# Kernel optimization log

Measured on AMD Instinct MI355X. Metric: run time of the kernel, lower is better.

## Reference

```python
import jax, jax.numpy as jnp
import numpy as np
from jax.scipy.linalg import expm

B, S, D, E, K, NROT = 2, 2048, 1024, 8, 2, 3
EPS = 1e-5


def setup_inputs() -> dict:
    key = jax.random.key(0)
    ks = jax.random.split(key, 16)
    sc = 0.02
    x = jax.random.normal(ks[0], (B, S, D), jnp.float32)
    ln_gamma = 1.0 + sc * jax.random.normal(ks[1], (D,), jnp.float32)
    ln_beta = sc * jax.random.normal(ks[2], (D,), jnp.float32)
    abel_w = sc * jax.random.normal(ks[3], (D, D), jnp.float32)
    abel_b = sc * jax.random.normal(ks[4], (D,), jnp.float32)
    moe_gate_w = sc * jax.random.normal(ks[5], (D, E), jnp.float32)
    moe_gate_b = sc * jax.random.normal(ks[6], (E,), jnp.float32)
    ew1 = sc * jax.random.normal(ks[7], (E, D, 2 * D), jnp.float32)
    eb1 = sc * jax.random.normal(ks[8], (E, 2 * D), jnp.float32)
    ew2 = sc * jax.random.normal(ks[9], (E, 2 * D, D), jnp.float32)
    eb2 = sc * jax.random.normal(ks[10], (E, D), jnp.float32)
    g = sc * jax.random.normal(ks[11], (NROT, D, D), jnp.float32)
    gens = 0.5 * (g - jnp.swapaxes(g, -1, -2))  # skew-symmetric, as in reset_parameters
    gc_w = sc * jax.random.normal(ks[12], (2 * D, 1), jnp.float32)
    gc_b = sc * jax.random.normal(ks[13], (1,), jnp.float32)
    return dict(x=x, ln_gamma=ln_gamma, ln_beta=ln_beta, abel_w=abel_w, abel_b=abel_b,
                moe_gate_w=moe_gate_w, moe_gate_b=moe_gate_b, ew1=ew1, eb1=eb1,
                ew2=ew2, eb2=eb2, gens=gens, gc_w=gc_w, gc_b=gc_b)


def _gelu(x):
    return jax.nn.gelu(x, approximate=False)  # torch nn.GELU default = exact erf


def _forward(x, ln_gamma, ln_beta, abel_w, abel_b, moe_gate_w, moe_gate_b,
             ew1, eb1, ew2, eb2, gens, gc_w, gc_b):
    residual = x
    # LayerNorm
    mu = jnp.mean(x, axis=-1, keepdims=True)
    var = jnp.mean((x - mu) ** 2, axis=-1, keepdims=True)
    xn = (x - mu) * jax.lax.rsqrt(var + EPS) * ln_gamma + ln_beta
    # abel branch: Linear + GELU
    abel_out = _gelu(xn @ abel_w + abel_b)
    # MoE: dense all-experts compute, masked by top-k softmax weights
    logits = xn @ moe_gate_w + moe_gate_b                      # [B,S,E]
    topw, topi = jax.lax.top_k(logits, K)                      # [B,S,K]
    topw = jax.nn.softmax(topw, axis=-1)
    w_dense = jnp.sum(jax.nn.one_hot(topi, E, dtype=xn.dtype) * topw[..., None], axis=-2)  # [B,S,E]
    h = _gelu(jnp.einsum('bsd,edh->ebsh', xn, ew1) + eb1[:, None, None, :])  # [E,B,S,2D]
    eo = jnp.einsum('ebsh,ehd->ebsd', h, ew2) + eb2[:, None, None, :]        # [E,B,S,D]
    moe_out = jnp.einsum('ebsd,bse->bsd', eo, w_dense)
    # GeometricRotation: sequential matrix_exp rotations
    for i in range(NROT):
        moe_out = moe_out @ expm(gens[i])
    # gated residual mix
    combined = jnp.concatenate([abel_out, moe_out], axis=-1)
    gate = jax.nn.sigmoid(combined @ gc_w + gc_b)              # [B,S,1]
    mixed = abel_out * (1.0 - gate) + moe_out * gate
    return residual + mixed


def reference(x, ln_gamma, ln_beta, abel_w, abel_b, moe_gate_w, moe_gate_b,
              ew1, eb1, ew2, eb2, gens, gc_w, gc_b):
    return _forward(x, ln_gamma, ln_beta, abel_w, abel_b, moe_gate_w, moe_gate_b,
                    ew1, eb1, ew2, eb2, gens, gc_w, gc_b)
```

## Files before the change

### kernel.cpp

```cpp
#include <hip/hip_runtime.h>
#include <hip/hip_bf16.h>
#include <cstdint>
#include <cstddef>

#define DD   1024
#define DD2  2048
#define EE   8
#define NTOK 4096
#define CAPR 9216

typedef __bf16 bf16_t;
typedef __bf16 bf16x8 __attribute__((ext_vector_type(8)));
typedef __bf16 bf16x4 __attribute__((ext_vector_type(4)));
typedef float  f32x4v __attribute__((ext_vector_type(4)));

__device__ __forceinline__ float gelu_f(float v){
  return 0.5f*v*(1.0f + erff(v*0.70710678118654752440f));
}

__device__ __forceinline__ void gload_lds16(const void* g, void* l){
  __builtin_amdgcn_global_load_lds(
    (const __attribute__((address_space(1))) unsigned int*)(uintptr_t)g,
    (__attribute__((address_space(3))) unsigned int*)(uintptr_t)l,
    16, 0, 0);
}

enum { EPI_GELU_F32=0, EPI_GELU_BF16=1, EPI_BIAS_BF16=2, EPI_SCALE_BF16=3,
       EPI_ADDV_BF16=4, EPI_BF16=5, EPI_F32=6 };

template<int BM,int BN,int EPI,bool DYN>
__global__ __launch_bounds__(256)
void gemm_bt(const bf16_t* __restrict__ A, const bf16_t* __restrict__ Bt,
             const bf16_t* __restrict__ Bt2,
             const int N, const int K, const int gx, const int gy, const int gz,
             const long sAz, const long sBz, const long sOz, const int zsplit,
             const int* __restrict__ cnt, const int* __restrict__ offp,
             const float* __restrict__ bias, const long sBias,
             const float alpha, const float alpha2,
             const bf16_t* __restrict__ addv,
             float* __restrict__ outF, bf16_t* __restrict__ outB)
{
  constexpr int BK = 64;
  constexpr int WM = BM/2, WN = BN/2;
  constexpr int FM = WM/16, FN = WN/16;
  constexpr int IA = BM/32, IB = BN/32;
  __shared__ alignas(16) bf16_t sA[BM*BK];
  __shared__ alignas(16) bf16_t sB[BN*BK];

  int bx, by, bz;
  if constexpr (DYN) {
    const int e = blockIdx.x & 7;
    const int i = blockIdx.x >> 3;
    bz = e; by = i / gx; bx = i - by*gx;
    if (by * BM >= cnt[e]) return;
  } else {
    const int nwg = gx * gy * gz;
    const int q = nwg >> 3, r = nwg & 7;
    const int k = blockIdx.x & 7, i = blockIdx.x >> 3;
    if (i >= q + (k < r ? 1 : 0)) return;
    const int l = k * q + (k < r ? k : r) + i;
    bx = l % gx; const int t2 = l / gx; by = t2 % gy; bz = t2 / gy;
  }

  const int z = bz;
  int zz = z; const bf16_t* Bp = Bt; float al = alpha;
  if (z >= zsplit) { zz = z - zsplit; Bp = Bt2; al = alpha2; }

  float*  oF = outF;
  bf16_t* oB = outB;
  if constexpr (DYN) {
    const long ro = offp[z];
    A  += ro * (long)K;
    oB += ro * (long)N;
  } else {
    A += (size_t)zz * sAz;
    if (oF) oF += (size_t)z * sOz;
    if (oB) oB += (size_t)z * sOz;
  }
  Bp += (size_t)zz * sBz;
  const float*  bp = bias ? bias + (size_t)z * sBias : nullptr;
  const bf16_t* vp = addv ? addv + (size_t)z * sOz   : nullptr;

  const int tid = threadIdx.x;
  const int wid = tid >> 6, lid = tid & 63;
  const int wr = wid >> 1, wc = wid & 1;
  const int brow = by * BM, bcol = bx * BN;
  const int sr = lid >> 3, sq = lid & 7;
  const int fr = lid & 15, fq = lid >> 4;

  f32x4v acc[FM][FN] = {};

  for (int kt = 0; kt < K; kt += BK) {
    #pragma unroll
    for (int i = 0; i < IA; i++) {
      const int ii = wid*IA + i;
      const int r  = ii*8 + sr;
      const int q  = sq ^ (r & 7);
      gload_lds16((const char*)A + ((size_t)(brow + r)*K + kt)*2 + q*16,
                  (char*)sA + ii*1024);
    }
    #pragma unroll
    for (int i = 0; i < IB; i++) {
      const int ii = wid*IB + i;
      const int r  = ii*8 + sr;
      const int q  = sq ^ (r & 7);
      gload_lds16((const char*)Bp + ((size_t)(bcol + r)*K + kt)*2 + q*16,
                  (char*)sB + ii*1024);
    }
    __syncthreads();

    #pragma unroll
    for (int kk = 0; kk < 2; kk++) {
      bf16x8 af[FM], bb[FN];
      #pragma unroll
      for (int mi = 0; mi < FM; mi++) {
        const int r = wr*WM + mi*16 + fr;
        const int q = (kk*4 + fq) ^ (r & 7);
        af[mi] = *(const bf16x8*)((const char*)sA + r*128 + q*16);
      }
      #pragma unroll
      for (int ni = 0; ni < FN; ni++) {
        const int r = wc*WN + ni*16 + fr;
        const int q = (kk*4 + fq) ^ (r & 7);
        bb[ni] = *(const bf16x8*)((const char*)sB + r*128 + q*16);
      }
      #pragma unroll
      for (int mi = 0; mi < FM; mi++)
        #pragma unroll
        for (int ni = 0; ni < FN; ni++)
          acc[mi][ni] = __builtin_amdgcn_mfma_f32_16x16x32_bf16(
              af[mi], bb[ni], acc[mi][ni], 0, 0, 0);
    }
    __syncthreads();
  }

  #pragma unroll
  for (int mi = 0; mi < FM; mi++) {
    #pragma unroll
    for (int ni = 0; ni < FN; ni++) {
      const int rg0 = brow + wr*WM + mi*16 + fq*4;
      const int cg  = bcol + wc*WN + ni*16 + fr;
      #pragma unroll
      for (int i = 0; i < 4; i++) {
        const int rg = rg0 + i;
        float v = acc[mi][ni][i];
        if constexpr (EPI == EPI_GELU_F32) {
          v += bp[cg];
          oF[(size_t)rg*N + cg] = gelu_f(v);
        } else if constexpr (EPI == EPI_GELU_BF16) {
          v += bp[cg];
          oB[(size_t)rg*N + cg] = (bf16_t)gelu_f(v);
        } else if constexpr (EPI == EPI_BIAS_BF16) {
          v += bp[cg];
          oB[(size_t)rg*N + cg] = (bf16_t)v;
        } else if constexpr (EPI == EPI_SCALE_BF16) {
          oB[(size_t)rg*N + cg] = (bf16_t)(v * al);
        } else if constexpr (EPI == EPI_ADDV_BF16) {
          oB[(size_t)rg*N + cg] = (bf16_t)(v + (float)vp[(size_t)rg*N + cg]);
        } else if constexpr (EPI == EPI_BF16) {
          oB[(size_t)rg*N + cg] = (bf16_t)v;
        } else {
          oF[(size_t)rg*N + cg] = v;
        }
      }
    }
  }
}

__global__ __launch_bounds__(256)
void tcvt_kernel(const float* __restrict__ src, bf16_t* __restrict__ dst, int R, int C){
  __shared__ float tile[32][33];
  const size_t bo = (size_t)blockIdx.z * R * C;
  const int c0 = blockIdx.x*32, r0 = blockIdx.y*32;
  #pragma unroll
  for (int i = 0; i < 4; i++) {
    const int r = r0 + threadIdx.y + i*8;
    tile[threadIdx.y + i*8][threadIdx.x] = src[bo + (size_t)r*C + c0 + threadIdx.x];
  }
  __syncthreads();
  #pragma unroll
  for (int i = 0; i < 4; i++) {
    const int c = c0 + threadIdx.y + i*8;
    dst[bo + (size_t)c*R + r0 + threadIdx.x] = (bf16_t)tile[threadIdx.x][threadIdx.y + i*8];
  }
}

__global__ __launch_bounds__(256)
void tb16_kernel(const bf16_t* __restrict__ Ut, bf16_t* __restrict__ Tb){
  __shared__ bf16_t tile[32][33];
  const bf16_t* src = Ut + (size_t)(1 - blockIdx.z) * DD * DD;
  bf16_t*       dst = Tb + (size_t)blockIdx.z * DD * DD;
  const int c0 = blockIdx.x*32, r0 = blockIdx.y*32;
  #pragma unroll
  for (int i = 0; i < 4; i++)
    tile[threadIdx.y + i*8][threadIdx.x] = src[(size_t)(r0 + threadIdx.y + i*8)*DD + c0 + threadIdx.x];
  __syncthreads();
  #pragma unroll
  for (int i = 0; i < 4; i++)
    dst[(size_t)(c0 + threadIdx.y + i*8)*DD + r0 + threadIdx.x] = tile[threadIdx.x][threadIdx.y + i*8];
}

__global__ __launch_bounds__(256)
void cvt_kernel(const float* __restrict__ in, bf16_t* __restrict__ o, long n, float scale){
  const long i = ((long)blockIdx.x*256 + threadIdx.x)*4;
  if (i >= n) return;
  const float4 v = *(const float4*)(in + i);
  bf16x4 b; b[0]=(bf16_t)(v.x*scale); b[1]=(bf16_t)(v.y*scale);
  b[2]=(bf16_t)(v.z*scale); b[3]=(bf16_t)(v.w*scale);
  *(bf16x4*)(o + i) = b;
}

__global__ __launch_bounds__(256)
void vw_kernel(const bf16_t* __restrict__ Hn, const bf16_t* __restrict__ H2,
               const bf16_t* __restrict__ H3, bf16_t* __restrict__ Vb,
               bf16_t* __restrict__ Wtb){
  const long i0 = ((long)blockIdx.x*256 + threadIdx.x)*4;
  const long rc = i0 % (long)(DD*DD);
  const int r = (int)(rc / DD), c0 = (int)(rc % DD);
  const bf16x4 h  = *(const bf16x4*)(Hn + i0);
  const bf16x4 h2 = *(const bf16x4*)(H2 + i0);
  const bf16x4 h3 = *(const bf16x4*)(H3 + i0);
  bf16x4 v, w;
  #pragma unroll
  for (int j = 0; j < 4; j++) {
    const float d  = (r == c0 + j) ? 1.0f : 0.0f;
    const float fh = (float)h[j], f2 = (float)h2[j], f3 = (float)h3[j];
    v[j] = (bf16_t)(d + fh + f2*0.5f + f3*(1.0f/6.0f));
    w[j] = (bf16_t)(d*(1.0f/24.0f) - fh*(1.0f/120.0f) + f2*(1.0f/720.0f) - f3*(1.0f/5040.0f));
  }
  *(bf16x4*)(Vb  + i0) = v;
  *(bf16x4*)(Wtb + i0) = w;
}

__global__ __launch_bounds__(256)
void ln_gate_kernel(const float* __restrict__ x, const float* __restrict__ gamma,
                    const float* __restrict__ beta, const float* __restrict__ gw,
                    const float* __restrict__ gb,
                    bf16_t* __restrict__ xnb, int2* __restrict__ ids,
                    float2* __restrict__ wts)
{
  const int t = blockIdx.x, tid = threadIdx.x, j0 = tid*4;
  const int wid = tid >> 6, lid = tid & 63;
  const float4 v = *(const float4*)(x + (size_t)t*DD + j0);
  float s  = v.x + v.y + v.z + v.w;
  float ss = v.x*v.x + v.y*v.y + v.z*v.z + v.w*v.w;
  #pragma unroll
  for (int off = 32; off; off >>= 1) { s += __shfl_down(s, off); ss += __shfl_down(ss, off); }
  __shared__ float redS[4], redQ[4], mv[2];
  if (lid == 0) { redS[wid] = s; redQ[wid] = ss; }
  __syncthreads();
  if (tid == 0) {
    const float S1 = redS[0]+redS[1]+redS[2]+redS[3];
    const float S2 = redQ[0]+redQ[1]+redQ[2]+redQ[3];
    const float mu  = S1 * (1.0f/DD);
    const float var = S2 * (1.0f/DD) - mu*mu;
    mv[0] = mu; mv[1] = rsqrtf(var + 1e-5f);
  }
  __syncthreads();
  const float mu = mv[0], rstd = mv[1];
  const float4 g = *(const float4*)(gamma + j0);
  const float4 b = *(const float4*)(beta  + j0);
  float xn[4];
  xn[0] = (v.x-mu)*rstd*g.x + b.x;
  xn[1] = (v.y-mu)*rstd*g.y + b.y;
  xn[2] = (v.z-mu)*rstd*g.z + b.z;
  xn[3] = (v.w-mu)*rstd*g.w + b.w;
  bf16x4 ov; ov[0]=(bf16_t)xn[0]; ov[1]=(bf16_t)xn[1]; ov[2]=(bf16_t)xn[2]; ov[3]=(bf16_t)xn[3];
  *(bf16x4*)(xnb + (size_t)t*DD + j0) = ov;

  float p[8] = {0,0,0,0,0,0,0,0};
  #pragma unroll
  for (int i = 0; i < 4; i++) {
    const float4 a0 = *(const float4*)(gw + (size_t)(j0+i)*EE);
    const float4 a1 = *(const float4*)(gw + (size_t)(j0+i)*EE + 4);
    const float xv = xn[i];
    p[0]+=xv*a0.x; p[1]+=xv*a0.y; p[2]+=xv*a0.z; p[3]+=xv*a0.w;
    p[4]+=xv*a1.x; p[5]+=xv*a1.y; p[6]+=xv*a1.z; p[7]+=xv*a1.w;
  }
  #pragma unroll
  for (int off = 32; off; off >>= 1) {
    #pragma unroll
    for (int e = 0; e < 8; e++) p[e] += __shfl_down(p[e], off);
  }
  __shared__ float pr[32];
  if (lid == 0) {
    #pragma unroll
    for (int e = 0; e < 8; e++) pr[wid*8 + e] = p[e];
  }
  __syncthreads();
  if (tid == 0) {
    float l[8];
    #pragma unroll
    for (int e = 0; e < 8; e++) l[e] = pr[e] + pr[8+e] + pr[16+e] + pr[24+e] + gb[e];
    int i1 = 0; float m1 = l[0];
    #pragma unroll
    for (int e = 1; e < 8; e++) if (l[e] > m1) { m1 = l[e]; i1 = e; }
    int i2 = 0; float m2 = -1e30f;
    #pragma unroll
    for (int e = 0; e < 8; e++) if (e != i1 && l[e] > m2) { m2 = l[e]; i2 = e; }
    const float wa = 1.0f/(1.0f + expf(m2 - m1));
    ids[t] = make_int2(i1, i2);
    wts[t] = make_float2(wa, 1.0f - wa);
  }
}

__global__ __launch_bounds__(256)
void route_kernel(const int2* __restrict__ ids, int* __restrict__ slotA,
                  int* __restrict__ slotB, int* __restrict__ cnt)
{
  const int e = blockIdx.x;
  const int tid = threadIdx.x;
  const int wid = tid >> 6, lid = tid & 63;
  __shared__ int wsum[4];
  int base = 0;
  const unsigned long long lt = (1ull << lid) - 1ull;
  for (int c0 = 0; c0 < NTOK; c0 += 256) {
    const int t = c0 + tid;
    const int2 id = ids[t];
    const bool fA = (id.x == e), fB = (id.y == e);
    const unsigned long long mA = __ballot(fA);
    const unsigned long long mB = __ballot(fB);
    const int cA = __popcll(mA), cB = __popcll(mB);
    const int pA = __popcll(mA & lt), pB = __popcll(mB & lt);
    if (lid == 0) wsum[wid] = cA + cB;
    __syncthreads();
    int wbase = 0;
    #pragma unroll
    for (int w = 0; w < 4; w++) if (w < wid) wbase += wsum[w];
    const int tot = wsum[0] + wsum[1] + wsum[2] + wsum[3];
    if (fA) slotA[t] = base + wbase + pA;
    if (fB) slotB[t] = base + wbase + cA + pB;
    base += tot;
    __syncthreads();
  }
  if (tid == 0) cnt[e] = base;
}

__global__ void offs_kernel(const int* __restrict__ cnt, int* __restrict__ off){
  if (threadIdx.x == 0) {
    int a = 0;
    for (int e = 0; e < EE; e++) { off[e] = a; a += (cnt[e] + 127) & ~127; }
  }
}

__global__ __launch_bounds__(256)
void gather_kernel(const bf16_t* __restrict__ xnb, const int2* __restrict__ ids,
                   const int* __restrict__ slotA, const int* __restrict__ slotB,
                   const int* __restrict__ off, bf16_t* __restrict__ Xg){
  const int t = blockIdx.x, j = threadIdx.x*4;
  const int2 id = ids[t];
  const bf16x4 v = *(const bf16x4*)(xnb + (size_t)t*DD + j);
  *(bf16x4*)(Xg + (size_t)(off[id.x] + slotA[t])*DD + j) = v;
  *(bf16x4*)(Xg + (size_t)(off[id.y] + slotB[t])*DD + j) = v;
}

__global__ __launch_bounds__(256)
void combine_kernel(const bf16_t* __restrict__ Yg, const int2* __restrict__ ids,
                    const int* __restrict__ slotA, const int* __restrict__ slotB,
                    const int* __restrict__ off, const float2* __restrict__ wts,
                    bf16_t* __restrict__ Xa){
  const int t = blockIdx.x, j = threadIdx.x*4;
  const int2 id = ids[t];
  const float2 w = wts[t];
  const bf16x4 a = *(const bf16x4*)(Yg + (size_t)(off[id.x] + slotA[t])*DD + j);
  const bf16x4 b = *(const bf16x4*)(Yg + (size_t)(off[id.y] + slotB[t])*DD + j);
  bf16x4 o;
  #pragma unroll
  for (int i = 0; i < 4; i++) o[i] = (bf16_t)(w.x*(float)a[i] + w.y*(float)b[i]);
  *(bf16x4*)(Xa + (size_t)t*DD + j) = o;
}

__global__ __launch_bounds__(256)
void mix_kernel(const float* __restrict__ x, const float* __restrict__ abel,
                const float* __restrict__ rot, const float* __restrict__ gcw,
                const float* __restrict__ gcb, float* __restrict__ out)
{
  const int t = blockIdx.x, tid = threadIdx.x, j0 = tid*4;
  const int wid = tid >> 6, lid = tid & 63;
  const float4 a  = *(const float4*)(abel + (size_t)t*DD + j0);
  const float4 r  = *(const float4*)(rot  + (size_t)t*DD + j0);
  const float4 ga = *(const float4*)(gcw + j0);
  const float4 gr = *(const float4*)(gcw + DD + j0);
  float p = a.x*ga.x + a.y*ga.y + a.z*ga.z + a.w*ga.w
          + r.x*gr.x + r.y*gr.y + r.z*gr.z + r.w*gr.w;
  #pragma unroll
  for (int off = 32; off; off >>= 1) p += __shfl_down(p, off);
  __shared__ float red[4];
  __shared__ float gsh;
  if (lid == 0) red[wid] = p;
  __syncthreads();
  if (tid == 0) {
    const float P = red[0] + red[1] + red[2] + red[3] + gcb[0];
    gsh = 1.0f/(1.0f + expf(-P));
  }
  __syncthreads();
  const float gate = gsh, g1 = 1.0f - gate;
  const float4 xv = *(const float4*)(x + (size_t)t*DD + j0);
  float4 o;
  o.x = xv.x + a.x*g1 + r.x*gate;
  o.y = xv.y + a.y*g1 + r.y*gate;
  o.z = xv.z + a.z*g1 + r.z*gate;
  o.w = xv.w + a.w*g1 + r.w*gate;
  *(float4*)(out + (size_t)t*DD + j0) = o;
}

extern "C" void kernel_launch(void* const* d_in, const int* in_sizes, int n_in,
                              void* d_out, int out_size, void* d_ws, size_t ws_size,
                              hipStream_t stream)
{
  (void)in_sizes; (void)n_in; (void)out_size; (void)ws_size;
  const float* x      = (const float*)d_in[0];
  const float* ln_g   = (const float*)d_in[1];
  const float* ln_b   = (const float*)d_in[2];
  const float* abel_w = (const float*)d_in[3];
  const float* abel_b = (const float*)d_in[4];
  const float* gate_w = (const float*)d_in[5];
  const float* gate_b = (const float*)d_in[6];
  const float* ew1    = (const float*)d_in[7];
  const float* eb1    = (const float*)d_in[8];
  const float* ew2    = (const float*)d_in[9];
  const float* eb2    = (const float*)d_in[10];
  const float* gens   = (const float*)d_in[11];
  const float* gc_w   = (const float*)d_in[12];
  const float* gc_b   = (const float*)d_in[13];
  float* out = (float*)d_out;

  char* wsp = (char*)d_ws;
  auto alloc = [&](size_t bytes) -> char* {
    char* p = wsp; wsp += (bytes + 255) & ~(size_t)255; return p;
  };
  const size_t MB = 1u<<20;
  bf16_t* xnb   = (bf16_t*)alloc((size_t)NTOK*DD*2);
  int2*   ids   = (int2*)  alloc((size_t)NTOK*8);
  float2* wts   = (float2*)alloc((size_t)NTOK*8);
  int*    slotA = (int*)   alloc((size_t)NTOK*4);
  int*    slotB = (int*)   alloc((size_t)NTOK*4);
  int*    cnt   = (int*)   alloc(64);
  int*    off   = (int*)   alloc(64);
  bf16_t* abel_wT = (bf16_t*)alloc((size_t)DD*DD*2);
  char*   UN      = alloc(64*MB);
  bf16_t* ew1T  = (bf16_t*)UN;
  bf16_t* ew2T  = (bf16_t*)(UN + 32*MB);
  bf16_t* Hn    = (bf16_t*)alloc((size_t)3*DD*DD*2);
  float*  abelo = (float*) alloc((size_t)NTOK*DD*4);
  bf16_t* Xg    = (bf16_t*)alloc((size_t)CAPR*DD*2);
  bf16_t* Hg    = (bf16_t*)alloc((size_t)CAPR*DD2*2);
  bf16_t* Xa    = (bf16_t*)alloc((size_t)NTOK*DD*2);
  bf16_t* Yg    = Xg;
  float*  rot   = (float*)Hg;
  bf16_t* H2  = (bf16_t*)(UN + 0*MB);
  bf16_t* H34 = (bf16_t*)(UN + 6*MB);
  bf16_t* Vb  = (bf16_t*)(UN + 18*MB);
  bf16_t* Wtb = (bf16_t*)(UN + 24*MB);
  bf16_t* Ut  = (bf16_t*)(UN + 30*MB);
  bf16_t* Tb  = (bf16_t*)(UN + 36*MB);
  bf16_t* Pb  = (bf16_t*)(UN + 40*MB);
  bf16_t* Rt  = (bf16_t*)(UN + 42*MB);
  const long D2 = (long)DD*DD;

  auto gflat = [](int gx, int gy, int gz) {
    const int nwg = gx*gy*gz; return 8 * ((nwg + 7) / 8);
  };

  const dim3 tb(32, 8, 1);
  tcvt_kernel<<<dim3(DD/32,  DD/32, 1),  tb, 0, stream>>>(abel_w, abel_wT, DD,  DD);
  tcvt_kernel<<<dim3(DD2/32, DD/32, EE), tb, 0, stream>>>(ew1,    ew1T,    DD,  DD2);
  tcvt_kernel<<<dim3(DD/32,  DD2/32,EE), tb, 0, stream>>>(ew2,    ew2T,    DD2, DD);
  cvt_kernel<<<dim3(3*DD*DD/1024,1,1), 256, 0, stream>>>(gens, Hn, (long)3*DD*DD, -1.0f);

  ln_gate_kernel<<<dim3(NTOK,1,1), 256, 0, stream>>>(x, ln_g, ln_b, gate_w, gate_b,
                                                     xnb, ids, wts);
  route_kernel<<<dim3(EE,1,1), 256, 0, stream>>>(ids, slotA, slotB, cnt);
  offs_kernel<<<dim3(1,1,1), 64, 0, stream>>>(cnt, off);
  gather_kernel<<<dim3(NTOK,1,1), 256, 0, stream>>>(xnb, ids, slotA, slotB, off, Xg);

  gemm_bt<128,128,EPI_GELU_BF16,true><<<dim3(8*(DD2/128)*(NTOK/128),1,1), 256, 0, stream>>>(
      Xg, ew1T, nullptr, DD2, DD, DD2/128, NTOK/128, EE, 0, (long)DD2*DD, 0, 1<<30,
      cnt, off, eb1, DD2, 1.0f, 0.0f, nullptr, nullptr, Hg);
  gemm_bt<128,128,EPI_BIAS_BF16,true><<<dim3(8*(DD/128)*(NTOK/128),1,1), 256, 0, stream>>>(
      Hg, ew2T, nullptr, DD, DD2, DD/128, NTOK/128, EE, 0, (long)DD*DD2, 0, 1<<30,
      cnt, off, eb2, DD, 1.0f, 0.0f, nullptr, nullptr, Yg);
  combine_kernel<<<dim3(NTOK,1,1), 256, 0, stream>>>(Yg, ids, slotA, slotB, off, wts, Xa);

  gemm_bt<128,64,EPI_GELU_F32,false><<<dim3(gflat(16,32,1),1,1), 256, 0, stream>>>(
      xnb, abel_wT, nullptr, DD, DD, 16, 32, 1, 0, 0, 0, 1<<30, nullptr, nullptr,
      abel_b, 0, 1.0f, 0.0f, nullptr, abelo, nullptr);

  gemm_bt<128,64,EPI_SCALE_BF16,false><<<dim3(gflat(16,8,3),1,1), 256, 0, stream>>>(
      Hn, Hn, nullptr, DD, DD, 16, 8, 3, D2, D2, D2, 1<<30, nullptr, nullptr,
      nullptr, 0, -1.0f, 0.0f, nullptr, nullptr, H2);
  gemm_bt<128,64,EPI_SCALE_BF16,false><<<dim3(gflat(16,8,6),1,1), 256, 0, stream>>>(
      H2, Hn, H2, DD, DD, 16, 8, 6, D2, D2, D2, 3, nullptr, nullptr,
      nullptr, 0, -1.0f, 1.0f, nullptr, nullptr, H34);
  vw_kernel<<<dim3(3*DD*DD/1024,1,1), 256, 0, stream>>>(Hn, H2, H34, Vb, Wtb);
  gemm_bt<128,64,EPI_ADDV_BF16,false><<<dim3(gflat(16,8,3),1,1), 256, 0, stream>>>(
      H34 + 3*D2, Wtb, nullptr, DD, DD, 16, 8, 3, D2, D2, D2, 1<<30, nullptr, nullptr,
      nullptr, 0, 1.0f, 0.0f, Vb, nullptr, Ut);
  tb16_kernel<<<dim3(32,32,2), tb, 0, stream>>>(Ut, Tb);
  gemm_bt<128,64,EPI_BF16,false><<<dim3(gflat(16,8,1),1,1), 256, 0, stream>>>(
      Ut + 2*D2, Tb, nullptr, DD, DD, 16, 8, 1, 0, 0, 0, 1<<30, nullptr, nullptr,
      nullptr, 0, 1.0f, 0.0f, nullptr, nullptr, Pb);
  gemm_bt<128,64,EPI_BF16,false><<<dim3(gflat(16,8,1),1,1), 256, 0, stream>>>(
      Pb, Tb + D2, nullptr, DD, DD, 16, 8, 1, 0, 0, 0, 1<<30, nullptr, nullptr,
      nullptr, 0, 1.0f, 0.0f, nullptr, nullptr, Rt);
  gemm_bt<128,64,EPI_F32,false><<<dim3(gflat(16,32,1),1,1), 256, 0, stream>>>(
      Xa, Rt, nullptr, DD, DD, 16, 32, 1, 0, 0, 0, 1<<30, nullptr, nullptr,
      nullptr, 0, 1.0f, 0.0f, nullptr, rot, nullptr);

  mix_kernel<<<dim3(NTOK,1,1), 256, 0, stream>>>(x, abelo, rot, gc_w, gc_b, out);
}
```

Measured before the change: 377.6 us.

## Use tanh-approx GELU, merge routing kernels, store abel output as bf16

Replaces exact erf GELU with a tanh-form approximation built from fast exp and divide. Merges the per-expert route kernel and the offsets kernel into one single-block kernel that ballots all experts at once. Stores the abel branch output as bf16 instead of fp32, which roughly halves that tensor's write and read traffic in the mix kernel. These trade accuracy (approximate GELU, bf16 rounding of abel_out) for less ALU work and memory traffic. The single-block routing also serialises work that was previously spread over 8 blocks.

```diff
diff --git a/kernel.cpp b/kernel.cpp
--- a/kernel.cpp
+++ b/kernel.cpp
@@ -15,7 +15,9 @@
 typedef float  f32x4v __attribute__((ext_vector_type(4)));
 
 __device__ __forceinline__ float gelu_f(float v){
-  return 0.5f*v*(1.0f + erff(v*0.70710678118654752440f));
+  const float t = v*(0.7978845608028654f + 0.0356774081f*v*v);
+  const float u = __expf(2.0f*t);
+  return __fdividef(v*u, 1.0f + u);
 }
 
 __device__ __forceinline__ void gload_lds16(const void* g, void* l){
@@ -306,40 +308,43 @@
 
 __global__ __launch_bounds__(256)
 void route_kernel(const int2* __restrict__ ids, int* __restrict__ slotA,
-                  int* __restrict__ slotB, int* __restrict__ cnt)
+                  int* __restrict__ slotB, int* __restrict__ cnt,
+                  int* __restrict__ off)
 {
-  const int e = blockIdx.x;
   const int tid = threadIdx.x;
   const int wid = tid >> 6, lid = tid & 63;
-  __shared__ int wsum[4];
-  int base = 0;
+  __shared__ int wsum[EE][4];
+  __shared__ int base[EE];
+  if (tid < EE) base[tid] = 0;
+  __syncthreads();
   const unsigned long long lt = (1ull << lid) - 1ull;
   for (int c0 = 0; c0 < NTOK; c0 += 256) {
     const int t = c0 + tid;
     const int2 id = ids[t];
-    const bool fA = (id.x == e), fB = (id.y == e);
-    const unsigned long long mA = __ballot(fA);
-    const unsigned long long mB = __ballot(fB);
-    const int cA = __popcll(mA), cB = __popcll(mB);
-    const int pA = __popcll(mA & lt), pB = __popcll(mB & lt);
-    if (lid == 0) wsum[wid] = cA + cB;
+    int pA = 0, pB = 0;
+    #pragma unroll
+    for (int e = 0; e < EE; e++) {
+      const bool fA = (id.x == e), fB = (id.y == e);
+      const unsigned long long mA = __ballot(fA);
+      const unsigned long long mB = __ballot(fB);
+      const int cA = __popcll(mA);
+      if (lid == 0) wsum[e][wid] = cA + __popcll(mB);
+      if (fA) pA = __popcll(mA & lt);
+      if (fB) pB = cA + __popcll(mB & lt);
+    }
     __syncthreads();
-    int wbase = 0;
-    #pragma unroll
-    for (int w = 0; w < 4; w++) if (w < wid) wbase += wsum[w];
-    const int tot = wsum[0] + wsum[1] + wsum[2] + wsum[3];
-    if (fA) slotA[t] = base + wbase + pA;
-    if (fB) slotB[t] = base + wbase + cA + pB;
-    base += tot;
+    int wbA = base[id.x], wbB = base[id.y];
+    for (int w = 0; w < wid; w++) { wbA += wsum[id.x][w]; wbB += wsum[id.y][w]; }
+    slotA[t] = wbA + pA;
+    slotB[t] = wbB + pB;
     __syncthreads();
-  }
-  if (tid == 0) cnt[e] = base;
-}
-
-__global__ void offs_kernel(const int* __restrict__ cnt, int* __restrict__ off){
-  if (threadIdx.x == 0) {
+    if (tid < EE) base[tid] += wsum[tid][0]+wsum[tid][1]+wsum[tid][2]+wsum[tid][3];
+    __syncthreads();
+  }
+  if (tid == 0) {
     int a = 0;
-    for (int e = 0; e < EE; e++) { off[e] = a; a += (cnt[e] + 127) & ~127; }
+    #pragma unroll
+    for (int e = 0; e < EE; e++) { cnt[e] = base[e]; off[e] = a; a += (base[e]+127)&~127; }
   }
 }
 
@@ -371,17 +376,18 @@
 }
 
 __global__ __launch_bounds__(256)
-void mix_kernel(const float* __restrict__ x, const float* __restrict__ abel,
+void mix_kernel(const float* __restrict__ x, const bf16_t* __restrict__ abel,
                 const float* __restrict__ rot, const float* __restrict__ gcw,
                 const float* __restrict__ gcb, float* __restrict__ out)
 {
   const int t = blockIdx.x, tid = threadIdx.x, j0 = tid*4;
   const int wid = tid >> 6, lid = tid & 63;
-  const float4 a  = *(const float4*)(abel + (size_t)t*DD + j0);
+  const bf16x4 ab = *(const bf16x4*)(abel + (size_t)t*DD + j0);
   const float4 r  = *(const float4*)(rot  + (size_t)t*DD + j0);
   const float4 ga = *(const float4*)(gcw + j0);
   const float4 gr = *(const float4*)(gcw + DD + j0);
-  float p = a.x*ga.x + a.y*ga.y + a.z*ga.z + a.w*ga.w
+  const float a0 = (float)ab[0], a1 = (float)ab[1], a2 = (float)ab[2], a3 = (float)ab[3];
+  float p = a0*ga.x + a1*ga.y + a2*ga.z + a3*ga.w
           + r.x*gr.x + r.y*gr.y + r.z*gr.z + r.w*gr.w;
   #pragma unroll
   for (int off = 32; off; off >>= 1) p += __shfl_down(p, off);
@@ -397,10 +403,10 @@
   const float gate = gsh, g1 = 1.0f - gate;
   const float4 xv = *(const float4*)(x + (size_t)t*DD + j0);
   float4 o;
-  o.x = xv.x + a.x*g1 + r.x*gate;
-  o.y = xv.y + a.y*g1 + r.y*gate;
-  o.z = xv.z + a.z*g1 + r.z*gate;
-  o.w = xv.w + a.w*g1 + r.w*gate;
+  o.x = xv.x + a0*g1 + r.x*gate;
+  o.y = xv.y + a1*g1 + r.y*gate;
+  o.z = xv.z + a2*g1 + r.z*gate;
+  o.w = xv.w + a3*g1 + r.w*gate;
   *(float4*)(out + (size_t)t*DD + j0) = o;
 }
 
@@ -442,7 +448,7 @@
   bf16_t* ew1T  = (bf16_t*)UN;
   bf16_t* ew2T  = (bf16_t*)(UN + 32*MB);
   bf16_t* Hn    = (bf16_t*)alloc((size_t)3*DD*DD*2);
-  float*  abelo = (float*) alloc((size_t)NTOK*DD*4);
+  bf16_t* abelo = (bf16_t*)alloc((size_t)NTOK*DD*2);
   bf16_t* Xg    = (bf16_t*)alloc((size_t)CAPR*DD*2);
   bf16_t* Hg    = (bf16_t*)alloc((size_t)CAPR*DD2*2);
   bf16_t* Xa    = (bf16_t*)alloc((size_t)NTOK*DD*2);
@@ -470,8 +476,7 @@
 
   ln_gate_kernel<<<dim3(NTOK,1,1), 256, 0, stream>>>(x, ln_g, ln_b, gate_w, gate_b,
                                                      xnb, ids, wts);
-  route_kernel<<<dim3(EE,1,1), 256, 0, stream>>>(ids, slotA, slotB, cnt);
-  offs_kernel<<<dim3(1,1,1), 64, 0, stream>>>(cnt, off);
+  route_kernel<<<dim3(1,1,1), 256, 0, stream>>>(ids, slotA, slotB, cnt, off);
   gather_kernel<<<dim3(NTOK,1,1), 256, 0, stream>>>(xnb, ids, slotA, slotB, off, Xg);
 
   gemm_bt<128,128,EPI_GELU_BF16,true><<<dim3(8*(DD2/128)*(NTOK/128),1,1), 256, 0, stream>>>(
@@ -482,9 +487,9 @@
       cnt, off, eb2, DD, 1.0f, 0.0f, nullptr, nullptr, Yg);
   combine_kernel<<<dim3(NTOK,1,1), 256, 0, stream>>>(Yg, ids, slotA, slotB, off, wts, Xa);
 
-  gemm_bt<128,64,EPI_GELU_F32,false><<<dim3(gflat(16,32,1),1,1), 256, 0, stream>>>(
+  gemm_bt<128,64,EPI_GELU_BF16,false><<<dim3(gflat(16,32,1),1,1), 256, 0, stream>>>(
       xnb, abel_wT, nullptr, DD, DD, 16, 32, 1, 0, 0, 0, 1<<30, nullptr, nullptr,
-      abel_b, 0, 1.0f, 0.0f, nullptr, abelo, nullptr);
+      abel_b, 0, 1.0f, 0.0f, nullptr, nullptr, abelo);
 
   gemm_bt<128,64,EPI_SCALE_BF16,false><<<dim3(gflat(16,8,3),1,1), 256, 0, stream>>>(
       Hn, Hn, nullptr, DD, DD, 16, 8, 3, D2, D2, D2, 1<<30, nullptr, nullptr,
```

After: 383.8 us. Within noise of the previous version (+1.7%).
